# Kernel optimization log

Measured on AMD Instinct MI355X. Metric: run time of the kernel, lower is better.

The kernel has to match this reference:

```python
import jax, jax.numpy as jnp
import numpy as np

B, NF, H = 1024, 64, 512


def setup_inputs() -> dict:
    key = jax.random.key(0)
    ks = jax.random.split(key, 12)
    sc_in2 = 1.0 / np.sqrt(2 * H)
    sc_in1 = 1.0 / np.sqrt(H)
    inp = {
        "field_vectors": jax.random.normal(ks[0], (B, NF, H), dtype=jnp.float32),
        # and_fusion: Linear(2H->H), ReLU, Linear(H->H)
        "and_W1": jax.random.uniform(ks[1], (2 * H, H), jnp.float32, -sc_in2, sc_in2),
        "and_b1": jax.random.uniform(ks[2], (H,), jnp.float32, -sc_in2, sc_in2),
        "and_W2": jax.random.uniform(ks[3], (H, H), jnp.float32, -sc_in1, sc_in1),
        "and_b2": jax.random.uniform(ks[4], (H,), jnp.float32, -sc_in1, sc_in1),
        # or_fusion: Linear(2H->H), ReLU, Linear(H->H)
        "or_W1": jax.random.uniform(ks[5], (2 * H, H), jnp.float32, -sc_in2, sc_in2),
        "or_b1": jax.random.uniform(ks[6], (H,), jnp.float32, -sc_in2, sc_in2),
        "or_W2": jax.random.uniform(ks[7], (H, H), jnp.float32, -sc_in1, sc_in1),
        "or_b2": jax.random.uniform(ks[8], (H,), jnp.float32, -sc_in1, sc_in1),
        # not_transform: Linear(H->H), Tanh
        "not_W": jax.random.uniform(ks[9], (H, H), jnp.float32, -sc_in1, sc_in1),
        "not_b": jax.random.uniform(ks[10], (H,), jnp.float32, -sc_in1, sc_in1),
        # Disjoint index structure so the torch skip-set logic is a no-op:
        # 'and' pairs use fields 0..31, 'or' pairs use 32..47, leftovers 48..63.
        "not_idx": 48 + jnp.arange(8, dtype=jnp.int32),
        "and_pairs": jnp.arange(32, dtype=jnp.int32).reshape(16, 2),
        "or_pairs": (32 + jnp.arange(16, dtype=jnp.int32)).reshape(8, 2),
        "leftover_idx": 48 + jnp.arange(16, dtype=jnp.int32),
    }
    return inp


def _mlp2(x, W1, b1, W2, b2):
    # Linear -> ReLU -> Linear
    return jax.nn.relu(x @ W1 + b1) @ W2 + b2


def reference(field_vectors, and_W1, and_b1, and_W2, and_b2,
              or_W1, or_b1, or_W2, or_b2, not_W, not_b,
              not_idx, and_pairs, or_pairs, leftover_idx):
    # In-place 'not' transform on selected fields (Tanh(Linear))
    fv = field_vectors.at[:, not_idx].set(
        jnp.tanh(field_vectors[:, not_idx] @ not_W + not_b))
    # Gather (i, j) pairs, concat along feature dim -> [B, P, 2H]
    cat_and = jnp.concatenate([fv[:, and_pairs[:, 0]], fv[:, and_pairs[:, 1]]], axis=-1)
    fused_and = _mlp2(cat_and, and_W1, and_b1, and_W2, and_b2)  # [B, 16, H]
    cat_or = jnp.concatenate([fv[:, or_pairs[:, 0]], fv[:, or_pairs[:, 1]]], axis=-1)
    fused_or = _mlp2(cat_or, or_W1, or_b1, or_W2, or_b2)  # [B, 8, H]
    # Stack order matches torch loop: and results, or results, untouched fields
    return jnp.concatenate([fused_and, fused_or, fv[:, leftover_idx]], axis=1)
```

## Files before the change

### kernel.cpp

```cpp
#include <hip/hip_runtime.h>
#include <hip/hip_bf16.h>
#include <math.h>

typedef __attribute__((ext_vector_type(8))) __bf16 bf16x8;
typedef __attribute__((ext_vector_type(4))) float f32x4;

__device__ __forceinline__ unsigned short f2bf(float f) {
    union { float f; unsigned u; } v; v.f = f;
    unsigned r = v.u + 0x7fffu + ((v.u >> 16) & 1u);
    return (unsigned short)(r >> 16);
}
__device__ __forceinline__ unsigned int pk(float a, float b) {
    union { float f; unsigned u; } x, y; x.f = a; y.f = b;
    unsigned ra = (x.u + 0x7fffu + ((x.u >> 16) & 1u)) >> 16;
    unsigned rb = (y.u + 0x7fffu + ((y.u >> 16) & 1u)) & 0xffff0000u;
    return ra | rb;
}

struct WArgs {
    const float* W[5];
    unsigned short* WT[5];
    int N[5];
    int tstart[6];
};

__global__ __launch_bounds__(256) void wprep_kernel(WArgs a) {
    __shared__ float tile[64][65];
    const int blk = blockIdx.x;
    const int tid = threadIdx.x;
    int m = 0;
    while (blk >= a.tstart[m + 1]) m++;
    const float* src = a.W[m];
    unsigned short* dst = a.WT[m];
    const int N = a.N[m];
    const int t = blk - a.tstart[m];
    const int ntn = N >> 6;
    const int tk = t / ntn, tn = t % ntn;
    const int c = tid & 63, r0 = tid >> 6;
    #pragma unroll
    for (int r = r0; r < 64; r += 4)
        tile[r][c] = src[(size_t)(tk * 64 + r) * N + tn * 64 + c];
    __syncthreads();
    const int l = tid & 63;
    #pragma unroll
    for (int fi = tid >> 6; fi < 8; fi += 4) {
        const int ktl = fi & 1, cgl = fi >> 1;
        const int kt = tk * 2 + ktl, cg = tn * 4 + cgl;
        const int kb = ktl * 32 + (l >> 4) * 8;
        const int nb = cgl * 16 + (l & 15);
        uint4 o;
        o.x = pk(tile[kb + 0][nb], tile[kb + 1][nb]);
        o.y = pk(tile[kb + 2][nb], tile[kb + 3][nb]);
        o.z = pk(tile[kb + 4][nb], tile[kb + 5][nb]);
        o.w = pk(tile[kb + 6][nb], tile[kb + 7][nb]);
        ((uint4*)dst)[((size_t)kt * 32 + cg) * 64 + l] = o;
    }
}

#define LOADB(DST, WTP, K0)                                                  \
    _Pragma("unroll") for (int ni = 0; ni < 4; ni++)                         \
        DST[ni] = *(const bf16x8*)((WTP) +                                   \
            ((((size_t)(K0) >> 5) * 32 + cg0 + ni) << 9) + (lane << 3));

#define MMAC(BF, AF)                                                         \
    _Pragma("unroll") for (int mi = 0; mi < 4; mi++)                         \
    _Pragma("unroll") for (int ni = 0; ni < 4; ni++)                         \
        acc[mi][ni] = __builtin_amdgcn_mfma_f32_16x16x32_bf16(               \
            AF[mi], BF[ni], acc[mi][ni], 0, 0, 0);

#define LBAR()                                                               \
    asm volatile("s_waitcnt lgkmcnt(0)" ::: "memory");                       \
    asm volatile("s_barrier" ::: "memory");

template <int P, int K1, int PATH, int QBASE>
__device__ __forceinline__ void fused_seg(
    const float* __restrict__ fv,
    const int* __restrict__ idx,
    const unsigned short* __restrict__ W1T,
    const float* __restrict__ b1,
    const unsigned short* __restrict__ W2T,
    const float* __restrict__ b2,
    float* __restrict__ out,
    const int* __restrict__ leftover,
    int local,
    unsigned short* As, unsigned short* hid) {

    const int tid  = threadIdx.x;
    const int lane = tid & 63, w = tid >> 6;
    const int ln15 = lane & 15;
    const int kq   = lane >> 4;
    const int wn   = w * 64;
    const int cg0  = w * 4;
    const int m0   = local * 64;
    constexpr int NTK = K1 / 32;

    const int r  = tid >> 3;
    const int ks = tid & 7;
    const float *ar0, *ar1;
    {
        const int m = m0 + r;
        if constexpr (PATH == 0) {
            const int b = m / P, p = m % P;
            ar0 = fv + ((size_t)b * 64 + idx[2 * p]) * 512 + ks * 4;
            ar1 = fv + ((size_t)b * 64 + idx[2 * p + 1]) * 512 + ks * 4;
        } else {
            const int b = m >> 3, i = m & 7;
            ar0 = fv + ((size_t)b * 64 + idx[i]) * 512 + ks * 4;
            ar1 = ar0;
        }
    }
    auto ldA = [&](int t) -> float4 {
        const int k0 = t * 32;
        if constexpr (K1 == 1024)
            return *(const float4*)(k0 >= 512 ? ar1 + (k0 - 512) : ar0 + k0);
        else
            return *(const float4*)(ar0 + k0);
    };
    unsigned short* const wdst =
        As + r * 32 + (((ks >> 1) ^ (r & 3)) << 3) + ((ks & 1) << 2);
    auto wrA = [&](int buf, float4 v) {
        uint2 o; o.x = pk(v.x, v.y); o.y = pk(v.z, v.w);
        *(uint2*)(wdst + buf * 2048) = o;
    };
    const int xsel = (kq ^ (lane & 3)) * 8;

    f32x4 acc[4][4];
    #pragma unroll
    for (int mi = 0; mi < 4; mi++)
        #pragma unroll
        for (int ni = 0; ni < 4; ni++)
            acc[mi][ni] = f32x4{0.f, 0.f, 0.f, 0.f};

    bf16x8 bA[4];

    float4 va = ldA(0);
    float4 vb = ldA(1);
    wrA(0, va);
    LBAR();

    for (int h = 0; h < NTK; h += 2) {
        {
            LOADB(bA, W1T, h * 32);
            if (h + 2 < NTK) va = ldA(h + 2);
            bf16x8 af[4];
            #pragma unroll
            for (int mi = 0; mi < 4; mi++)
                af[mi] = *(const bf16x8*)&As[(mi * 16 + ln15) * 32 + xsel];
            MMAC(bA, af);
            wrA(1, vb);
            LBAR();
        }
        {
            LOADB(bA, W1T, (h + 1) * 32);
            if (h + 3 < NTK) vb = ldA(h + 3);
            bf16x8 af[4];
            #pragma unroll
            for (int mi = 0; mi < 4; mi++)
                af[mi] = *(const bf16x8*)&As[2048 + (mi * 16 + ln15) * 32 + xsel];
            MMAC(bA, af);
            if (h + 2 < NTK) { wrA(0, va); }
            LBAR();
        }
    }

    if constexpr (PATH == 2) {
        int qmap[8];
        #pragma unroll
        for (int i = 0; i < 8; i++) {
            const int f = idx[i];
            int q = 24;
            for (int l = 0; l < 16; l++)
                if (leftover[l] == f) q = 24 + l;
            qmap[i] = q;
        }
        #pragma unroll
        for (int ni = 0; ni < 4; ni++) {
            const int n = wn + ni * 16 + ln15;
            const float bv = b1[n];
            #pragma unroll
            for (int mi = 0; mi < 4; mi++)
                #pragma unroll
                for (int j = 0; j < 4; j++) {
                    const int rr = mi * 16 + kq * 4 + j;
                    const int m = m0 + rr;
                    const int b = m >> 3, i = m & 7;
                    out[((size_t)b * 40 + qmap[i]) * 512 + n] =
                        tanhf(acc[mi][ni][j] + bv);
                }
        }
        return;
    }

    #pragma unroll
    for (int ni = 0; ni < 4; ni++) {
        const int n  = wn + ni * 16 + ln15;
        const float bv = b1[n];
        const int c8 = n >> 3;
        const int cl = (n & 7) * 2;
        #pragma unroll
        for (int mi = 0; mi < 4; mi++)
            #pragma unroll
            for (int j = 0; j < 4; j++) {
                const int rr = mi * 16 + kq * 4 + j;
                float v = acc[mi][ni][j] + bv;
                v = v > 0.f ? v : 0.f;
                *(unsigned short*)((char*)hid + rr * 1024 +
                                   ((c8 ^ (rr & 7)) * 16) + cl) = f2bf(v);
            }
    }
    #pragma unroll
    for (int mi = 0; mi < 4; mi++)
        #pragma unroll
        for (int ni = 0; ni < 4; ni++)
            acc[mi][ni] = f32x4{0.f, 0.f, 0.f, 0.f};
    __syncthreads();

    for (int t2 = 0; t2 < 16; t2++) {
        LOADB(bA, W2T, t2 * 32);
        bf16x8 af[4];
        #pragma unroll
        for (int mi = 0; mi < 4; mi++) {
            const int rr = mi * 16 + ln15;
            const int c8 = t2 * 4 + kq;
            af[mi] = *(const bf16x8*)((char*)hid + rr * 1024 +
                                      ((c8 ^ (rr & 7)) * 16));
        }
        MMAC(bA, af);
    }

    #pragma unroll
    for (int ni = 0; ni < 4; ni++) {
        const int n  = wn + ni * 16 + ln15;
        const float bv = b2[n];
        #pragma unroll
        for (int mi = 0; mi < 4; mi++)
            #pragma unroll
            for (int j = 0; j < 4; j++) {
                const int rr = mi * 16 + kq * 4 + j;
                const int m = m0 + rr;
                const int b = m / P, p = m % P;
                out[((size_t)b * 40 + QBASE + p) * 512 + n] =
                    acc[mi][ni][j] + bv;
            }
    }
}

struct FArgs {
    const float* fv;
    const unsigned short *and_W1T, *and_W2T, *or_W1T, *or_W2T, *not_WT;
    const int *and_pairs, *or_pairs, *not_idx, *leftover;
    const float *and_b1, *and_b2, *or_b1, *or_b2, *not_b;
    float* out;
};

__global__ __launch_bounds__(512, 4) void fused_phase(FArgs a) {
    __shared__ __align__(16) unsigned short As[2 * 64 * 32];
    __shared__ __align__(16) unsigned short hid[64 * 512];
    const int blk = blockIdx.x;
    if (blk < 256) {
        fused_seg<16, 1024, 0, 0>(a.fv, a.and_pairs, a.and_W1T, a.and_b1,
                                  a.and_W2T, a.and_b2, a.out, nullptr,
                                  blk, As, hid);
    } else if (blk < 384) {
        fused_seg<8, 1024, 0, 16>(a.fv, a.or_pairs, a.or_W1T, a.or_b1,
                                  a.or_W2T, a.or_b2, a.out, nullptr,
                                  blk - 256, As, hid);
    } else if (blk < 512) {
        fused_seg<8, 512, 2, 24>(a.fv, a.not_idx, a.not_WT, a.not_b,
                                 nullptr, nullptr, a.out, a.leftover,
                                 blk - 384, As, hid);
    } else {
        const int t = (blk - 512) * 512 + threadIdx.x;
        const size_t e = (size_t)t * 8;
        const int c  = (int)(e & 511);
        const int ls = (int)((e >> 9) & 15);
        const int b  = (int)(e >> 13);
        const int f  = a.leftover[ls];
        int isnot = 0;
        #pragma unroll
        for (int i = 0; i < 8; i++) isnot |= (a.not_idx[i] == f);
        if (isnot) return;
        const float* s = a.fv + ((size_t)b * 64 + f) * 512 + c;
        float* d = a.out + ((size_t)b * 40 + 24 + ls) * 512 + c;
        *(float4*)(d)     = *(const float4*)(s);
        *(float4*)(d + 4) = *(const float4*)(s + 4);
    }
}

extern "C" void kernel_launch(void* const* d_in, const int* in_sizes, int n_in,
                              void* d_out, int out_size, void* d_ws, size_t ws_size,
                              hipStream_t stream) {
    const float* fv       = (const float*)d_in[0];
    const float* and_W1   = (const float*)d_in[1];
    const float* and_b1   = (const float*)d_in[2];
    const float* and_W2   = (const float*)d_in[3];
    const float* and_b2   = (const float*)d_in[4];
    const float* or_W1    = (const float*)d_in[5];
    const float* or_b1    = (const float*)d_in[6];
    const float* or_W2    = (const float*)d_in[7];
    const float* or_b2    = (const float*)d_in[8];
    const float* not_W    = (const float*)d_in[9];
    const float* not_b    = (const float*)d_in[10];
    const int* not_idx    = (const int*)d_in[11];
    const int* and_pairs  = (const int*)d_in[12];
    const int* or_pairs   = (const int*)d_in[13];
    const int* leftover   = (const int*)d_in[14];
    float* out = (float*)d_out;
    char* ws = (char*)d_ws;

    unsigned short* and_W1T = (unsigned short*)(ws);
    unsigned short* or_W1T  = (unsigned short*)(ws + 1048576);
    unsigned short* and_W2T = (unsigned short*)(ws + 2097152);
    unsigned short* or_W2T  = (unsigned short*)(ws + 2621440);
    unsigned short* not_WT  = (unsigned short*)(ws + 3145728);

    WArgs wa;
    wa.W[0] = and_W1; wa.WT[0] = and_W1T; wa.N[0] = 512;
    wa.W[1] = or_W1;  wa.WT[1] = or_W1T;  wa.N[1] = 512;
    wa.W[2] = and_W2; wa.WT[2] = and_W2T; wa.N[2] = 512;
    wa.W[3] = or_W2;  wa.WT[3] = or_W2T;  wa.N[3] = 512;
    wa.W[4] = not_W;  wa.WT[4] = not_WT;  wa.N[4] = 512;
    wa.tstart[0] = 0;   wa.tstart[1] = 128; wa.tstart[2] = 256;
    wa.tstart[3] = 320; wa.tstart[4] = 384; wa.tstart[5] = 448;
    wprep_kernel<<<dim3(448), dim3(256), 0, stream>>>(wa);

    FArgs fa;
    fa.fv = fv;
    fa.and_W1T = and_W1T; fa.and_W2T = and_W2T;
    fa.or_W1T = or_W1T;   fa.or_W2T = or_W2T;   fa.not_WT = not_WT;
    fa.and_pairs = and_pairs; fa.or_pairs = or_pairs; fa.not_idx = not_idx;
    fa.leftover = leftover;
    fa.and_b1 = and_b1; fa.and_b2 = and_b2;
    fa.or_b1 = or_b1;   fa.or_b2 = or_b2;   fa.not_b = not_b;
    fa.out = out;
    fused_phase<<<dim3(512 + 2048), dim3(512), 0, stream>>>(fa);
}
```

Measured before the change: 308.1 us.

## Double-buffer weight fragments in GEMM loops and move leftover copy to prep kernel

```diff
diff --git a/kernel.cpp b/kernel.cpp
--- a/kernel.cpp
+++ b/kernel.cpp
@@ -18,6 +18,9 @@
 }
 
 struct WArgs {
+    const float* fv;
+    const int *not_idx, *leftover;
+    float* out;
     const float* W[5];
     unsigned short* WT[5];
     int N[5];
@@ -28,6 +31,25 @@
     __shared__ float tile[64][65];
     const int blk = blockIdx.x;
     const int tid = threadIdx.x;
+
+    if (blk >= 448) {
+        const int t = (blk - 448) * 256 + tid;
+        const size_t e = (size_t)t * 8;
+        const int c  = (int)(e & 511);
+        const int ls = (int)((e >> 9) & 15);
+        const int b  = (int)(e >> 13);
+        const int f  = a.leftover[ls];
+        int isnot = 0;
+        #pragma unroll
+        for (int i = 0; i < 8; i++) isnot |= (a.not_idx[i] == f);
+        if (isnot) return;
+        const float* s = a.fv + ((size_t)b * 64 + f) * 512 + c;
+        float* d = a.out + ((size_t)b * 40 + 24 + ls) * 512 + c;
+        *(float4*)(d)     = *(const float4*)(s);
+        *(float4*)(d + 4) = *(const float4*)(s + 4);
+        return;
+    }
+
     int m = 0;
     while (blk >= a.tstart[m + 1]) m++;
     const float* src = a.W[m];
@@ -71,6 +93,11 @@
 #define LBAR()                                                               \
     asm volatile("s_waitcnt lgkmcnt(0)" ::: "memory");                       \
     asm volatile("s_barrier" ::: "memory");
+
+#define AFRD(AF, BUF)                                                        \
+    _Pragma("unroll") for (int mi = 0; mi < 4; mi++)                         \
+        AF[mi] = *(const bf16x8*)&As[(BUF) * 2048 +                          \
+                                     (mi * 16 + ln15) * 32 + xsel];
 
 template <int P, int K1, int PATH, int QBASE>
 __device__ __forceinline__ void fused_seg(
@@ -131,36 +158,39 @@
         for (int ni = 0; ni < 4; ni++)
             acc[mi][ni] = f32x4{0.f, 0.f, 0.f, 0.f};
 
-    bf16x8 bA[4];
-
-    float4 va = ldA(0);
-    float4 vb = ldA(1);
-    wrA(0, va);
+    bf16x8 bA[4], bB[4];
+
+    float4 v0 = ldA(0), v1 = ldA(1), v2 = ldA(2), v3 = ldA(3);
+    LOADB(bA, W1T, 0);
+    wrA(0, v0);
     LBAR();
 
-    for (int h = 0; h < NTK; h += 2) {
-        {
-            LOADB(bA, W1T, h * 32);
-            if (h + 2 < NTK) va = ldA(h + 2);
-            bf16x8 af[4];
-            #pragma unroll
-            for (int mi = 0; mi < 4; mi++)
-                af[mi] = *(const bf16x8*)&As[(mi * 16 + ln15) * 32 + xsel];
-            MMAC(bA, af);
-            wrA(1, vb);
-            LBAR();
-        }
-        {
-            LOADB(bA, W1T, (h + 1) * 32);
-            if (h + 3 < NTK) vb = ldA(h + 3);
-            bf16x8 af[4];
-            #pragma unroll
-            for (int mi = 0; mi < 4; mi++)
-                af[mi] = *(const bf16x8*)&As[2048 + (mi * 16 + ln15) * 32 + xsel];
-            MMAC(bA, af);
-            if (h + 2 < NTK) { wrA(0, va); }
-            LBAR();
-        }
+    for (int h = 0; h < NTK; h += 4) {
+        bf16x8 af[4];
+        LOADB(bB, W1T, (h + 1) * 32);
+        if (h + 4 < NTK) v0 = ldA(h + 4);
+        AFRD(af, 0);
+        MMAC(bA, af);
+        wrA(1, v1);
+        LBAR();
+        LOADB(bA, W1T, (h + 2) * 32);
+        if (h + 5 < NTK) v1 = ldA(h + 5);
+        AFRD(af, 1);
+        MMAC(bB, af);
+        wrA(0, v2);
+        LBAR();
+        LOADB(bB, W1T, (h + 3) * 32);
+        if (h + 6 < NTK) v2 = ldA(h + 6);
+        AFRD(af, 0);
+        MMAC(bA, af);
+        wrA(1, v3);
+        LBAR();
+        if (h + 4 < NTK) { LOADB(bA, W1T, (h + 4) * 32); }
+        if (h + 7 < NTK) v3 = ldA(h + 7);
+        AFRD(af, 1);
+        MMAC(bB, af);
+        if (h + 4 < NTK) { wrA(0, v0); }
+        LBAR();
     }
 
     if constexpr (PATH == 2) {
@@ -215,9 +245,10 @@
             acc[mi][ni] = f32x4{0.f, 0.f, 0.f, 0.f};
     __syncthreads();
 
-    for (int t2 = 0; t2 < 16; t2++) {
-        LOADB(bA, W2T, t2 * 32);
+    LOADB(bA, W2T, 0);
+    for (int t2 = 0; t2 < 16; t2 += 2) {
         bf16x8 af[4];
+        LOADB(bB, W2T, (t2 + 1) * 32);
         #pragma unroll
         for (int mi = 0; mi < 4; mi++) {
             const int rr = mi * 16 + ln15;
@@ -226,6 +257,15 @@
                                       ((c8 ^ (rr & 7)) * 16));
         }
         MMAC(bA, af);
+        if (t2 + 2 < 16) { LOADB(bA, W2T, (t2 + 2) * 32); }
+        #pragma unroll
+        for (int mi = 0; mi < 4; mi++) {
+            const int rr = mi * 16 + ln15;
+            const int c8 = (t2 + 1) * 4 + kq;
+            af[mi] = *(const bf16x8*)((char*)hid + rr * 1024 +
+                                      ((c8 ^ (rr & 7)) * 16));
+        }
+        MMAC(bB, af);
     }
 
     #pragma unroll
@@ -265,25 +305,10 @@
         fused_seg<8, 1024, 0, 16>(a.fv, a.or_pairs, a.or_W1T, a.or_b1,
                                   a.or_W2T, a.or_b2, a.out, nullptr,
                                   blk - 256, As, hid);
-    } else if (blk < 512) {
+    } else {
         fused_seg<8, 512, 2, 24>(a.fv, a.not_idx, a.not_WT, a.not_b,
                                  nullptr, nullptr, a.out, a.leftover,
                                  blk - 384, As, hid);
-    } else {
-        const int t = (blk - 512) * 512 + threadIdx.x;
-        const size_t e = (size_t)t * 8;
-        const int c  = (int)(e & 511);
-        const int ls = (int)((e >> 9) & 15);
-        const int b  = (int)(e >> 13);
-        const int f  = a.leftover[ls];
-        int isnot = 0;
-        #pragma unroll
-        for (int i = 0; i < 8; i++) isnot |= (a.not_idx[i] == f);
-        if (isnot) return;
-        const float* s = a.fv + ((size_t)b * 64 + f) * 512 + c;
-        float* d = a.out + ((size_t)b * 40 + 24 + ls) * 512 + c;
-        *(float4*)(d)     = *(const float4*)(s);
-        *(float4*)(d + 4) = *(const float4*)(s + 4);
     }
 }
 
@@ -315,6 +340,8 @@
     unsigned short* not_WT  = (unsigned short*)(ws + 3145728);
 
     WArgs wa;
+    wa.fv = fv; wa.out = out;
+    wa.not_idx = not_idx; wa.leftover = leftover;
     wa.W[0] = and_W1; wa.WT[0] = and_W1T; wa.N[0] = 512;
     wa.W[1] = or_W1;  wa.WT[1] = or_W1T;  wa.N[1] = 512;
     wa.W[2] = and_W2; wa.WT[2] = and_W2T; wa.N[2] = 512;
@@ -322,7 +349,7 @@
     wa.W[4] = not_W;  wa.WT[4] = not_WT;  wa.N[4] = 512;
     wa.tstart[0] = 0;   wa.tstart[1] = 128; wa.tstart[2] = 256;
     wa.tstart[3] = 320; wa.tstart[4] = 384; wa.tstart[5] = 448;
-    wprep_kernel<<<dim3(448), dim3(256), 0, stream>>>(wa);
+    wprep_kernel<<<dim3(448 + 4096), dim3(256), 0, stream>>>(wa);
 
     FArgs fa;
     fa.fv = fv;
@@ -333,5 +360,5 @@
     fa.and_b1 = and_b1; fa.and_b2 = and_b2;
     fa.or_b1 = or_b1;   fa.or_b2 = or_b2;   fa.not_b = not_b;
     fa.out = out;
-    fused_phase<<<dim3(512 + 2048), dim3(512), 0, stream>>>(fa);
-}
+    fused_phase<<<dim3(512), dim3(512), 0, stream>>>(fa);
+}
```

Result: slower. 334.8 us (+8.7%).
